# Optimization experiments

Measured on AMD Instinct MI355X. Metric: run time of the kernel, lower is better.

Reference implementation:

```python
import jax, jax.numpy as jnp
import numpy as np

# Dims chosen per init_kwargs / input_specs. Note: the original module's reshapes
# are only numel-consistent when seq_len == d_model, so S == D here.
B, S, D, H, K = 16, 1024, 1024, 8, 3
PAD = (K - 1) // 2


def setup_inputs() -> dict:
    key = jax.random.key(0)
    k1, k2, k3, k4, k5 = jax.random.split(key, 5)
    query_sequences = jax.random.normal(k1, (B, S, D), jnp.float32)
    key_sequences = jax.random.normal(k2, (B, S, D), jnp.float32)
    value_sequences = jax.random.normal(k3, (B, S, D), jnp.float32)  # unused by forward (faithful)
    key_value_sequence_lengths = jax.random.randint(k4, (B,), 1, S + 1, jnp.int32)
    # cast_queries = nn.Linear(d_model, n_heads * kernel_size)
    Wq = jax.random.normal(k5, (D, H * K), jnp.float32) / np.sqrt(D).astype(np.float32)
    bq = jnp.zeros((H * K,), jnp.float32)
    conv_bias = jnp.zeros((H,), jnp.float32)  # self.conv_bias, initialized to zeros
    return {
        "query_sequences": query_sequences,
        "key_sequences": key_sequences,
        "value_sequences": value_sequences,
        "Wq": Wq,
        "bq": bq,
        "conv_bias": conv_bias,
        "key_value_sequence_lengths": key_value_sequence_lengths,
    }


def reference(query_sequences, key_sequences, value_sequences, Wq, bq, conv_bias,
              key_value_sequence_lengths):
    # weights = cast_queries(q): (B, S, H*K); buffer reinterpreted as per-batch
    # grouped-conv kernels (B, H, D, K)  [valid since S == D]
    w = (query_sequences @ Wq + bq).reshape(B, H, D, K)
    x = key_sequences.transpose(0, 2, 1)  # (B, D, S): channels-first keys

    # Per-example conv: groups=batch emulated by vmapping a dense conv1d
    # (in_channels=D, out_channels=H, kernel=K, padding=(K-1)//2) over the batch.
    def conv_one(xb, wb):  # xb: (D, S), wb: (H, D, K)
        y = jax.lax.conv_general_dilated(
            xb[None], wb, window_strides=(1,), padding=[(PAD, PAD)],
            dimension_numbers=("NCH", "OIH", "NCH"))
        return y[0]  # (H, S)

    out = jax.vmap(conv_one)(x, w) + conv_bias[None, :, None]  # (B, H, S)
    return out
```

## Files before the change

kernel.cpp:

```cpp
#include <hip/hip_runtime.h>
#include <cstdint>

constexpr int B_  = 16;
constexpr int S_  = 1024;
constexpr int D_  = 1024;
constexpr int H_  = 8;
constexpr int NJ  = 24;
constexpr int TR  = 64;
constexpr int DD  = 128;
constexpr int ND2 = DD / 2;
constexpr int NCH = D_ / DD;
constexpr int XPITCH = 66;

typedef _Float16 h2_t __attribute__((ext_vector_type(2)));

static __device__ __forceinline__ uint32_t packh2(float a, float b) {
  union { h2_t h; uint32_t u; } cv;
  cv.h[0] = (_Float16)a;
  cv.h[1] = (_Float16)b;
  return cv.u;
}

static __device__ __forceinline__ float dot2(uint32_t a, uint32_t b, float c) {
  union { uint32_t u; h2_t h; } ca, cb;
  ca.u = a; cb.u = b;
#if __has_builtin(__builtin_amdgcn_fdot2)
  return __builtin_amdgcn_fdot2(ca.h, cb.h, c, false);
#else
  return c + (float)ca.h[0] * (float)cb.h[0] + (float)ca.h[1] * (float)cb.h[1];
#endif
}

template <int MODE>
__global__ __launch_bounds__(256)
void skinny_gemm(const float* __restrict__ X, const float* __restrict__ W,
                 const float* __restrict__ bias, float* __restrict__ out)
{
  __shared__ uint32_t Xp[TR][XPITCH];
  __shared__ uint32_t Wp[ND2][NJ];

  const int b   = blockIdx.x >> 4;
  const int s0  = (blockIdx.x & 15) * TR;
  const int tid = threadIdx.x;
  const int cg  = tid & 7;
  const int rg  = tid >> 3;

  const float* Xb = X + (size_t)b * S_ * D_;
  const float* Wb = (MODE == 0) ? W : (W + (size_t)b * D_ * NJ);

  int xrow[8], xc4[8];
#pragma unroll
  for (int p = 0; p < 8; ++p) {
    int t4 = p * 256 + tid;
    xrow[p] = t4 >> 5;
    xc4[p]  = t4 & 31;
  }
  int wd2[6], wj[6];
#pragma unroll
  for (int i = 0; i < 6; ++i) {
    int idx = i * 256 + tid;
    wd2[i] = idx / 24;
    wj[i]  = idx % 24;
  }

  float4 xr[8];
  float  wra[6], wrb[6];

  auto stage_load = [&](int d0) {
#pragma unroll
    for (int p = 0; p < 8; ++p)
      xr[p] = *(const float4*)(Xb + (size_t)(s0 + xrow[p]) * D_ + d0 + xc4[p] * 4);
#pragma unroll
    for (int i = 0; i < 6; ++i) {
      const float* wp = Wb + (size_t)(d0 + 2 * wd2[i]) * NJ + wj[i];
      wra[i] = wp[0];
      wrb[i] = wp[NJ];
    }
  };
  auto stage_write = [&]() {
#pragma unroll
    for (int p = 0; p < 8; ++p) {
      uint32_t lo = packh2(xr[p].x, xr[p].y);
      uint32_t hi = packh2(xr[p].z, xr[p].w);
      *(uint2*)&Xp[xrow[p]][2 * xc4[p]] = make_uint2(lo, hi);
    }
#pragma unroll
    for (int i = 0; i < 6; ++i)
      Wp[wd2[i]][wj[i]] = packh2(wra[i], wrb[i]);
  };

  float acc[2][3] = {{0.f, 0.f, 0.f}, {0.f, 0.f, 0.f}};

  stage_load(0);
  stage_write();
  __syncthreads();

  for (int k = 0; k < NCH; ++k) {
    if (k + 1 < NCH) stage_load((k + 1) * DD);
#pragma unroll 8
    for (int d2 = 0; d2 < ND2; ++d2) {
      uint32_t x0 = Xp[2 * rg][d2];
      uint32_t x1 = Xp[2 * rg + 1][d2];
      uint32_t w0 = Wp[d2][3 * cg];
      uint32_t w1 = Wp[d2][3 * cg + 1];
      uint32_t w2 = Wp[d2][3 * cg + 2];
      acc[0][0] = dot2(x0, w0, acc[0][0]);
      acc[0][1] = dot2(x0, w1, acc[0][1]);
      acc[0][2] = dot2(x0, w2, acc[0][2]);
      acc[1][0] = dot2(x1, w0, acc[1][0]);
      acc[1][1] = dot2(x1, w1, acc[1][1]);
      acc[1][2] = dot2(x1, w2, acc[1][2]);
    }
    __syncthreads();
    if (k + 1 < NCH) {
      stage_write();
      __syncthreads();
    }
  }

  if (MODE == 0) {
#pragma unroll
    for (int r = 0; r < 2; ++r) {
      int s = s0 + 2 * rg + r;
      int h = s >> 7;
      int d = (s & 127) * 8 + cg;
      float* dst = out + ((size_t)b * D_ + d) * NJ + h * 3;
#pragma unroll
      for (int i = 0; i < 3; ++i)
        dst[i] = acc[r][i] + bias[3 * cg + i];
    }
  } else {
#pragma unroll
    for (int r = 0; r < 2; ++r) {
      int t = s0 + 2 * rg + r;
      float* dst = out + ((size_t)b * S_ + t) * NJ + 3 * cg;
#pragma unroll
      for (int i = 0; i < 3; ++i)
        dst[i] = acc[r][i];
    }
  }
}

__global__ __launch_bounds__(256)
void conv_combine(const float* __restrict__ U, const float* __restrict__ cbias,
                  float* __restrict__ out)
{
  __shared__ float Ul[258][25];
  const int b   = blockIdx.x >> 2;
  const int s0  = (blockIdx.x & 3) * 256;
  const int tid = threadIdx.x;

#pragma unroll
  for (int i = 0; i < 25; ++i) {
    int idx = i * 256 + tid;
    if (idx < 258 * 24) {
      int row = idx / 24;
      int p   = idx % 24;
      int t   = s0 - 1 + row;
      float v = 0.f;
      if (t >= 0 && t < S_) v = U[((size_t)b * S_ + t) * NJ + p];
      Ul[row][p] = v;
    }
  }
  __syncthreads();

  const int s = s0 + tid;
#pragma unroll
  for (int h = 0; h < H_; ++h) {
    float v = Ul[tid][3 * h] + Ul[tid + 1][3 * h + 1] + Ul[tid + 2][3 * h + 2] + cbias[h];
    out[((size_t)(b * H_ + h)) * S_ + s] = v;
  }
}

extern "C" void kernel_launch(void* const* d_in, const int* in_sizes, int n_in,
                              void* d_out, int out_size, void* d_ws, size_t ws_size,
                              hipStream_t stream)
{
  const float* Q   = (const float*)d_in[0];
  const float* Key = (const float*)d_in[1];
  const float* Wq  = (const float*)d_in[3];
  const float* bq  = (const float*)d_in[4];
  const float* cb  = (const float*)d_in[5];
  float* out = (float*)d_out;

  float* Wfilt = (float*)d_ws;
  float* U     = Wfilt + (size_t)B_ * D_ * NJ;

  skinny_gemm<0><<<B_ * (S_ / TR), 256, 0, stream>>>(Q, Wq, bq, Wfilt);
  skinny_gemm<1><<<B_ * (S_ / TR), 256, 0, stream>>>(Key, Wfilt, nullptr, U);
  conv_combine<<<B_ * (S_ / 256), 256, 0, stream>>>(U, cb, out);
}
```

Baseline: 213.2 us.

## Use MFMA f16 matrix cores and split-K across two blocks for skinny GEMMs

Replaces the packed fdot2 inner loop with 16x16x32 f16 MFMA instructions over a transposed weight tile, and splits the reduction dimension in half so each GEMM launches twice as many blocks writing two partial outputs. The second GEMM sums the two partial filter buffers while staging, and the combine kernel sums the two partial U buffers. This targets the low occupancy and scalar dot-product throughput of the bandwidth-bound skinny GEMMs, at the cost of extra workspace traffic for partial sums and wasted MFMA columns (24 of 32 used).

```diff
diff --git a/kernel.cpp b/kernel.cpp
--- a/kernel.cpp
+++ b/kernel.cpp
@@ -1,149 +1,145 @@
 #include <hip/hip_runtime.h>
 #include <cstdint>
 
-constexpr int B_  = 16;
-constexpr int S_  = 1024;
-constexpr int D_  = 1024;
-constexpr int H_  = 8;
-constexpr int NJ  = 24;
-constexpr int TR  = 64;
-constexpr int DD  = 128;
-constexpr int ND2 = DD / 2;
-constexpr int NCH = D_ / DD;
-constexpr int XPITCH = 66;
+constexpr int B_ = 16, S_ = 1024, D_ = 1024, H_ = 8, NJ = 24;
+constexpr int BM     = 64;
+constexpr int KC     = 128;
+constexpr int KHALF  = 512;
+constexpr int NCHUNK = KHALF / KC;
+constexpr int XPIT   = 136;
 
-typedef _Float16 h2_t __attribute__((ext_vector_type(2)));
+typedef _Float16 f16x8 __attribute__((ext_vector_type(8)));
+typedef float    f32x4 __attribute__((ext_vector_type(4)));
 
 static __device__ __forceinline__ uint32_t packh2(float a, float b) {
-  union { h2_t h; uint32_t u; } cv;
+  union { _Float16 h[2]; uint32_t u; } cv;
   cv.h[0] = (_Float16)a;
   cv.h[1] = (_Float16)b;
   return cv.u;
 }
 
-static __device__ __forceinline__ float dot2(uint32_t a, uint32_t b, float c) {
-  union { uint32_t u; h2_t h; } ca, cb;
-  ca.u = a; cb.u = b;
-#if __has_builtin(__builtin_amdgcn_fdot2)
-  return __builtin_amdgcn_fdot2(ca.h, cb.h, c, false);
-#else
-  return c + (float)ca.h[0] * (float)cb.h[0] + (float)ca.h[1] * (float)cb.h[1];
-#endif
-}
+template <int MODE>
+__global__ __launch_bounds__(256, 2)
+void gemm16(const float* __restrict__ X, const float* __restrict__ Wsrc0,
+            const float* __restrict__ Wsrc1, const float* __restrict__ bias,
+            float* __restrict__ P0, float* __restrict__ P1)
+{
+  __shared__ alignas(16) _Float16 Xt[BM][XPIT];
+  __shared__ alignas(16) _Float16 Wt[32][XPIT];
 
-template <int MODE>
-__global__ __launch_bounds__(256)
-void skinny_gemm(const float* __restrict__ X, const float* __restrict__ W,
-                 const float* __restrict__ bias, float* __restrict__ out)
-{
-  __shared__ uint32_t Xp[TR][XPITCH];
-  __shared__ uint32_t Wp[ND2][NJ];
+  const int tid  = threadIdx.x;
+  const int bid  = blockIdx.x;
+  const int half = bid & 1;
+  const int rt   = (bid >> 1) & 15;
+  const int b    = bid >> 5;
+  const int s0   = rt * BM;
+  const int k0g  = half * KHALF;
 
-  const int b   = blockIdx.x >> 4;
-  const int s0  = (blockIdx.x & 15) * TR;
-  const int tid = threadIdx.x;
-  const int cg  = tid & 7;
-  const int rg  = tid >> 3;
-
-  const float* Xb = X + (size_t)b * S_ * D_;
-  const float* Wb = (MODE == 0) ? W : (W + (size_t)b * D_ * NJ);
-
-  int xrow[8], xc4[8];
-#pragma unroll
-  for (int p = 0; p < 8; ++p) {
-    int t4 = p * 256 + tid;
-    xrow[p] = t4 >> 5;
-    xc4[p]  = t4 & 31;
-  }
-  int wd2[6], wj[6];
-#pragma unroll
-  for (int i = 0; i < 6; ++i) {
-    int idx = i * 256 + tid;
-    wd2[i] = idx / 24;
-    wj[i]  = idx % 24;
-  }
+  const float* Xb = X + ((size_t)b * S_ + s0) * D_;
+  const float* Wb0 = (MODE == 0) ? Wsrc0 : Wsrc0 + (size_t)b * D_ * NJ;
+  const float* Wb1 = (MODE == 0) ? nullptr : Wsrc1 + (size_t)b * D_ * NJ;
 
   float4 xr[8];
-  float  wra[6], wrb[6];
+  float  wA0[6], wA1[6];
+  float  wB0[6], wB1[6];
 
-  auto stage_load = [&](int d0) {
+  auto stage_load = [&](int kc) {
+    const int k0 = k0g + kc * KC;
 #pragma unroll
-    for (int p = 0; p < 8; ++p)
-      xr[p] = *(const float4*)(Xb + (size_t)(s0 + xrow[p]) * D_ + d0 + xc4[p] * 4);
+    for (int it = 0; it < 8; ++it) {
+      int f4 = it * 256 + tid;
+      xr[it] = *(const float4*)(Xb + (size_t)(f4 >> 5) * D_ + k0 + (f4 & 31) * 4);
+    }
 #pragma unroll
-    for (int i = 0; i < 6; ++i) {
-      const float* wp = Wb + (size_t)(d0 + 2 * wd2[i]) * NJ + wj[i];
-      wra[i] = wp[0];
-      wrb[i] = wp[NJ];
+    for (int it = 0; it < 6; ++it) {
+      int flat = it * 256 + tid;
+      int kp = flat / 24, j = flat - kp * 24;
+      const float* p0 = Wb0 + (size_t)(k0 + 2 * kp) * NJ + j;
+      wA0[it] = p0[0]; wA1[it] = p0[NJ];
+      if (MODE == 1) {
+        const float* p1 = Wb1 + (size_t)(k0 + 2 * kp) * NJ + j;
+        wB0[it] = p1[0]; wB1[it] = p1[NJ];
+      }
     }
   };
   auto stage_write = [&]() {
 #pragma unroll
-    for (int p = 0; p < 8; ++p) {
-      uint32_t lo = packh2(xr[p].x, xr[p].y);
-      uint32_t hi = packh2(xr[p].z, xr[p].w);
-      *(uint2*)&Xp[xrow[p]][2 * xc4[p]] = make_uint2(lo, hi);
+    for (int it = 0; it < 8; ++it) {
+      int f4 = it * 256 + tid;
+      int row = f4 >> 5, c4 = f4 & 31;
+      uint2 v = make_uint2(packh2(xr[it].x, xr[it].y), packh2(xr[it].z, xr[it].w));
+      *(uint2*)&Xt[row][c4 * 4] = v;
     }
 #pragma unroll
-    for (int i = 0; i < 6; ++i)
-      Wp[wd2[i]][wj[i]] = packh2(wra[i], wrb[i]);
+    for (int it = 0; it < 6; ++it) {
+      int flat = it * 256 + tid;
+      int kp = flat / 24, j = flat - kp * 24;
+      float a = wA0[it], c = wA1[it];
+      if (MODE == 1) { a += wB0[it]; c += wB1[it]; }
+      *(uint32_t*)&Wt[j][2 * kp] = packh2(a, c);
+    }
   };
 
-  float acc[2][3] = {{0.f, 0.f, 0.f}, {0.f, 0.f, 0.f}};
+  const int lane = tid & 63, w = tid >> 6;
+  const int arow = 16 * w + (lane & 15);
+  const int kgrp = ((lane >> 4) & 3) * 8;
+  const int colA = lane & 15;
+
+  f32x4 acc0 = {0.f, 0.f, 0.f, 0.f};
+  f32x4 acc1 = {0.f, 0.f, 0.f, 0.f};
+
+  for (int idx = tid; idx < 544; idx += 256) ((uint32_t*)&Wt[24][0])[idx] = 0u;
 
   stage_load(0);
   stage_write();
   __syncthreads();
 
-  for (int k = 0; k < NCH; ++k) {
-    if (k + 1 < NCH) stage_load((k + 1) * DD);
-#pragma unroll 8
-    for (int d2 = 0; d2 < ND2; ++d2) {
-      uint32_t x0 = Xp[2 * rg][d2];
-      uint32_t x1 = Xp[2 * rg + 1][d2];
-      uint32_t w0 = Wp[d2][3 * cg];
-      uint32_t w1 = Wp[d2][3 * cg + 1];
-      uint32_t w2 = Wp[d2][3 * cg + 2];
-      acc[0][0] = dot2(x0, w0, acc[0][0]);
-      acc[0][1] = dot2(x0, w1, acc[0][1]);
-      acc[0][2] = dot2(x0, w2, acc[0][2]);
-      acc[1][0] = dot2(x1, w0, acc[1][0]);
-      acc[1][1] = dot2(x1, w1, acc[1][1]);
-      acc[1][2] = dot2(x1, w2, acc[1][2]);
+  for (int c = 0; c < NCHUNK; ++c) {
+    if (c + 1 < NCHUNK) stage_load(c + 1);
+#pragma unroll
+    for (int ks = 0; ks < KC / 32; ++ks) {
+      f16x8 a  = *(const f16x8*)&Xt[arow][ks * 32 + kgrp];
+      f16x8 b0 = *(const f16x8*)&Wt[colA][ks * 32 + kgrp];
+      f16x8 b1 = *(const f16x8*)&Wt[colA + 16][ks * 32 + kgrp];
+      acc0 = __builtin_amdgcn_mfma_f32_16x16x32_f16(a, b0, acc0, 0, 0, 0);
+      acc1 = __builtin_amdgcn_mfma_f32_16x16x32_f16(a, b1, acc1, 0, 0, 0);
     }
     __syncthreads();
-    if (k + 1 < NCH) {
-      stage_write();
-      __syncthreads();
-    }
+    if (c + 1 < NCHUNK) { stage_write(); __syncthreads(); }
   }
 
+  float* Pdst = (half == 0) ? P0 : P1;
+  const int rbase = s0 + 16 * w + ((lane >> 4) & 3) * 4;
+
   if (MODE == 0) {
+    const int j0 = colA, j1 = 16 + colA;
+    const int jd0 = j0 / 3, jm0 = j0 - 3 * jd0;
+    const int jd1 = j1 / 3, jm1 = j1 - 3 * jd1;
+    const float bj0 = (half == 0) ? bias[j0] : 0.f;
+    const float bj1 = (half == 0 && colA < 8) ? bias[j1] : 0.f;
+    float* Pb_ = Pdst + (size_t)b * D_ * NJ;
 #pragma unroll
-    for (int r = 0; r < 2; ++r) {
-      int s = s0 + 2 * rg + r;
-      int h = s >> 7;
-      int d = (s & 127) * 8 + cg;
-      float* dst = out + ((size_t)b * D_ + d) * NJ + h * 3;
-#pragma unroll
-      for (int i = 0; i < 3; ++i)
-        dst[i] = acc[r][i] + bias[3 * cg + i];
+    for (int r = 0; r < 4; ++r) {
+      int s = rbase + r;
+      int h = s >> 7, sl = s & 127;
+      Pb_[(size_t)(sl * 8 + jd0) * NJ + 3 * h + jm0] = acc0[r] + bj0;
+      if (colA < 8)
+        Pb_[(size_t)(sl * 8 + jd1) * NJ + 3 * h + jm1] = acc1[r] + bj1;
     }
   } else {
+    float* Ub_ = Pdst + (size_t)b * S_ * NJ;
 #pragma unroll
-    for (int r = 0; r < 2; ++r) {
-      int t = s0 + 2 * rg + r;
-      float* dst = out + ((size_t)b * S_ + t) * NJ + 3 * cg;
-#pragma unroll
-      for (int i = 0; i < 3; ++i)
-        dst[i] = acc[r][i];
+    for (int r = 0; r < 4; ++r) {
+      int t = rbase + r;
+      Ub_[(size_t)t * NJ + colA] = acc0[r];
+      if (colA < 8) Ub_[(size_t)t * NJ + 16 + colA] = acc1[r];
     }
   }
 }
 
 __global__ __launch_bounds__(256)
-void conv_combine(const float* __restrict__ U, const float* __restrict__ cbias,
-                  float* __restrict__ out)
+void conv_combine(const float* __restrict__ Ua, const float* __restrict__ Ub,
+                  const float* __restrict__ cbias, float* __restrict__ out)
 {
   __shared__ float Ul[258][25];
   const int b   = blockIdx.x >> 2;
@@ -158,7 +154,10 @@
       int p   = idx % 24;
       int t   = s0 - 1 + row;
       float v = 0.f;
-      if (t >= 0 && t < S_) v = U[((size_t)b * S_ + t) * NJ + p];
+      if (t >= 0 && t < S_) {
+        size_t a = ((size_t)b * S_ + t) * NJ + p;
+        v = Ua[a] + Ub[a];
+      }
       Ul[row][p] = v;
     }
   }
@@ -183,10 +182,12 @@
   const float* cb  = (const float*)d_in[5];
   float* out = (float*)d_out;
 
-  float* Wfilt = (float*)d_ws;
-  float* U     = Wfilt + (size_t)B_ * D_ * NJ;
+  float* Pa = (float*)d_ws;
+  float* Pb = Pa + (size_t)B_ * D_ * NJ;
+  float* Ua = Pb + (size_t)B_ * D_ * NJ;
+  float* Ub = Ua + (size_t)B_ * S_ * NJ;
 
-  skinny_gemm<0><<<B_ * (S_ / TR), 256, 0, stream>>>(Q, Wq, bq, Wfilt);
-  skinny_gemm<1><<<B_ * (S_ / TR), 256, 0, stream>>>(Key, Wfilt, nullptr, U);
-  conv_combine<<<B_ * (S_ / 256), 256, 0, stream>>>(U, cb, out);
+  gemm16<0><<<512, 256, 0, stream>>>(Q,   Wq, nullptr, bq, Pa, Pb);
+  gemm16<1><<<512, 256, 0, stream>>>(Key, Pa, Pb, nullptr, Ua, Ub);
+  conv_combine<<<B_ * (S_ / 256), 256, 0, stream>>>(Ua, Ub, cb, out);
 }
```

Result: faster. 197.6 us (-7.3%).
